# Kernel optimization log

Hardware: AMD Instinct MI355X
Metric: run time of the kernel (lower is better)

## Reference

```python
import jax, jax.numpy as jnp
import numpy as np

N, NFEAT, NHID, NCLASS, NHEADS = 8192, 512, 64, 16, 4
ALPHA = 0.2          # leaky_relu slope for attention scores
OUT_SLOPE = 0.01     # flax default slope for per-head output leaky_relu
NEG = -9000000000000000.0


def glorot(key, shape):
    fan_in, fan_out = shape[0], shape[1]
    lim = jnp.sqrt(6.0 / (fan_in + fan_out))
    return jax.random.uniform(key, shape, jnp.float32, -lim, lim)


def setup_inputs() -> dict:
    key = jax.random.key(0)
    ks = jax.random.split(key, 6)
    x = jax.random.normal(ks[0], (N, NFEAT), jnp.float32)
    adj = jax.random.randint(ks[1], (N, N), 0, 2, jnp.int32)
    Wh = glorot(ks[2], (NHEADS * NFEAT, NHID)).reshape(NHEADS, NFEAT, NHID)
    ah = glorot(ks[3], (NHEADS * 2 * NHID, 1)).reshape(NHEADS, 2 * NHID, 1)
    Wo = glorot(ks[4], (NHID * NHEADS, NCLASS))
    ao = glorot(ks[5], (2 * NCLASS, 1))
    return {"x": x, "adj": adj, "Wh": Wh, "ah": ah, "Wo": Wo, "ao": ao}


def _gat_layer(x, adj_mask, W, a, score_slope):
    # h: (N, F)
    h = x @ W
    F = h.shape[1]
    # a_input[i,j] = concat(h_i, h_j); a_input @ a == f1[i] + f2[j]
    f1 = h @ a[:F, 0]   # (N,)
    f2 = h @ a[F:, 0]   # (N,)
    e = jax.nn.leaky_relu(f1[:, None] + f2[None, :], negative_slope=score_slope)
    att = jax.nn.softmax(jnp.where(adj_mask, e, NEG), axis=1)  # (N, N)
    return att @ h  # (N, F)


def reference(x, adj, Wh, ah, Wo, ao):
    adj_mask = adj > 0
    heads = []
    for k in range(NHEADS):  # small fixed structural loop
        hp = _gat_layer(x, adj_mask, Wh[k], ah[k], ALPHA)
        heads.append(jax.nn.leaky_relu(hp, negative_slope=OUT_SLOPE))
    xcat = jnp.concatenate(heads, axis=1)  # (N, NHEADS*NHID)
    # output head: concat=False -> return h_prime directly
    return _gat_layer(xcat, adj_mask, Wo, ao, ALPHA)  # (N, NCLASS)
```

## Files before the change

kernel.cpp:

```cpp
#include <hip/hip_runtime.h>
#include <stdint.h>

#define N      8192
#define FEAT   512
#define HID    64
#define NH     4
#define C1     256
#define PCH    65
#define TC     260
#define NCLS   16
#define C2     32
#define IPB    8
#define LOG2E  1.44269504f

typedef __attribute__((ext_vector_type(8))) short bf16x8;
typedef __attribute__((ext_vector_type(4))) float f32x4;

__device__ __forceinline__ float b2f(uint16_t u){
  uint32_t x = ((uint32_t)u) << 16;
  return __builtin_bit_cast(float, x);
}
__device__ __forceinline__ uint16_t f2b(float f){
  uint32_t x = __builtin_bit_cast(uint32_t, f);
  uint32_t r = (x + 0x7fffu + ((x >> 16) & 1u)) >> 16;
  return (uint16_t)r;
}
__device__ __forceinline__ float lrelu(float v, float a){ return fmaxf(v, a * v); }
__device__ __forceinline__ float fexp2(float x){
#if __has_builtin(__builtin_amdgcn_exp2f)
  return __builtin_amdgcn_exp2f(x);
#else
  return exp2f(x);
#endif
}
__device__ __forceinline__ uint32_t pk_bf16(float lo, float hi){
  uint32_t r;
  asm("v_cvt_pk_bf16_f32 %0, %1, %2" : "=v"(r) : "v"(lo), "v"(hi));
  return r;
}

__device__ __forceinline__ bf16x8 mk_frag(float f1v, float4 fa, float4 fb,
                                          uint32_t ub, float& dsum){
  float e0, e1, e2, e3, e4, e5, e6, e7, s;
  s = f1v + fa.x; e0 = fexp2(fmaxf(s, 0.2f * s)); if (!(ub &   1u)) e0 = 0.f;
  s = f1v + fa.y; e1 = fexp2(fmaxf(s, 0.2f * s)); if (!(ub &   2u)) e1 = 0.f;
  s = f1v + fa.z; e2 = fexp2(fmaxf(s, 0.2f * s)); if (!(ub &   4u)) e2 = 0.f;
  s = f1v + fa.w; e3 = fexp2(fmaxf(s, 0.2f * s)); if (!(ub &   8u)) e3 = 0.f;
  s = f1v + fb.x; e4 = fexp2(fmaxf(s, 0.2f * s)); if (!(ub &  16u)) e4 = 0.f;
  s = f1v + fb.y; e5 = fexp2(fmaxf(s, 0.2f * s)); if (!(ub &  32u)) e5 = 0.f;
  s = f1v + fb.z; e6 = fexp2(fmaxf(s, 0.2f * s)); if (!(ub &  64u)) e6 = 0.f;
  s = f1v + fb.w; e7 = fexp2(fmaxf(s, 0.2f * s)); if (!(ub & 128u)) e7 = 0.f;
  dsum += ((e0 + e1) + (e2 + e3)) + ((e4 + e5) + (e6 + e7));
  union { uint32_t u[4]; bf16x8 v; } r;
  r.u[0] = pk_bf16(e0, e1);
  r.u[1] = pk_bf16(e2, e3);
  r.u[2] = pk_bf16(e4, e5);
  r.u[3] = pk_bf16(e6, e7);
  return r.v;
}

#define MFMA16(a, b, c) __builtin_amdgcn_mfma_f32_16x16x32_bf16((a), (b), (c), 0, 0, 0)

__global__ __launch_bounds__(256) void kp_pack(const int* __restrict__ adj,
                                               uint32_t* __restrict__ adjT){
  __shared__ uint32_t tile[2][64];
  int t = threadIdx.x, lane = t & 63, wv = t >> 6;
  int jt = blockIdx.x & 127;
  int i0 = (blockIdx.x >> 7) * 64;
  const int j0 = jt * 64;
  #pragma unroll
  for (int r = 0; r < 16; ++r){
    int row = wv * 16 + r;
    unsigned long long mb = __ballot(adj[(size_t)(i0 + row) * N + j0 + lane] > 0);
    if (lane == 0){
      tile[0][row] = (uint32_t)mb;
      tile[1][row] = (uint32_t)(mb >> 32);
    }
  }
  __syncthreads();
  if (t < 128){
    int ww = t >> 6, r = t & 63;
    adjT[(size_t)(jt * 2 + ww) * N + i0 + r] = tile[ww][r];
  }
}

__global__ __launch_bounds__(256) void k1_h(const float* __restrict__ x,
    const float* __restrict__ Wh, const float* __restrict__ ah,
    uint16_t* __restrict__ H, float* __restrict__ f1, float* __restrict__ f2)
{
  int t = threadIdx.x;
  int i0 = blockIdx.x * IPB;
  int k = t >> 6, cc = t & 63;
  const float* wcol = Wh + k * 32768 + cc;
  float acc[IPB] = {};
  for (int f = 0; f < FEAT; f += 4){
    float w0 = wcol[(f + 0) * 64];
    float w1 = wcol[(f + 1) * 64];
    float w2 = wcol[(f + 2) * 64];
    float w3 = wcol[(f + 3) * 64];
    #pragma unroll
    for (int ii = 0; ii < IPB; ++ii){
      const float* xr = x + (size_t)(i0 + ii) * FEAT + f;
      acc[ii] += xr[0] * w0 + xr[1] * w1 + xr[2] * w2 + xr[3] * w3;
    }
  }
  float a1 = ah[k * 128 + cc], a2 = ah[k * 128 + 64 + cc];
  #pragma unroll
  for (int ii = 0; ii < IPB; ++ii){
    int i = i0 + ii;
    H[(size_t)i * C1 + t] = f2b(acc[ii]);
    float c1v = acc[ii] * a1, c2v = acc[ii] * a2;
    #pragma unroll
    for (int off = 32; off; off >>= 1){
      c1v += __shfl_down(c1v, off);
      c2v += __shfl_down(c2v, off);
    }
    if (cc == 0){ f1[k * N + i] = c1v * LOG2E; f2[k * N + i] = c2v * LOG2E; }
  }
}

__global__ void k2a_pack(const uint16_t* __restrict__ H, uint16_t* __restrict__ Bp){
  __shared__ uint16_t tile[64][72];
  int bid = blockIdx.x;
  int k = bid & 3, it = bid >> 2;
  int i0 = it * 64;
  int t = threadIdx.x;
  #pragma unroll
  for (int r = 0; r < 4; ++r){
    int ii = r * 16 + (t >> 4);
    int pp = (t & 15) * 4;
    uint2 v = *(const uint2*)(H + (size_t)(i0 + ii) * C1 + k * 64 + pp);
    const uint16_t* s = (const uint16_t*)&v;
    tile[pp + 0][ii] = s[0]; tile[pp + 1][ii] = s[1];
    tile[pp + 2][ii] = s[2]; tile[pp + 3][ii] = s[3];
  }
  __syncthreads();
  #pragma unroll
  for (int r = 0; r < 2; ++r){
    int jl = r;
    int ct = t >> 6;
    int lane = t & 63;
    int m = lane & 15, q = lane >> 4;
    uint4 v = *(const uint4*)&tile[ct * 16 + m][jl * 32 + q * 8];
    size_t off = ((((size_t)k * 256 + (i0 >> 5) + jl) * 4 + ct) * 64 + lane) * 8;
    *(uint4*)(Bp + off) = v;
  }
}

#define K3_LOADB(BD, JC)                                                        \
  { const int jb = (JC) & 63;                                                   \
    _Pragma("unroll")                                                           \
    for (int ct = 0; ct < 4; ++ct)                                              \
      BD[ct] = *(const bf16x8*)(bpbase + (size_t)(jb * 4 + ct) * 512); }

#define K3_LOADWF(W0d, W1d, F0d, F1d, JC)                                       \
  { const int jw = (JC) & 63;                                                   \
    W0d = adjT[awbase + (size_t)jw * N];                                        \
    W1d = adjT[awbase + (size_t)jw * N + 16];                                   \
    F0d = *(const float4*)(f2js + jw * 32 + 8 * q);                             \
    F1d = *(const float4*)(f2js + jw * 32 + 8 * q + 4); }

#define K3_COMP(BU, W0u, W1u, F0u, F1u)                                         \
  { bf16x8 af0 = mk_frag(f1v0, F0u, F1u, (W0u >> (8 * q)) & 255u, dsum0);       \
    bf16x8 af1 = mk_frag(f1v1, F0u, F1u, (W1u >> (8 * q)) & 255u, dsum1);       \
    _Pragma("unroll")                                                           \
    for (int ct = 0; ct < 4; ++ct){                                             \
      acc[0][ct] = MFMA16(af0, BU[ct], acc[0][ct]);                             \
      acc[1][ct] = MFMA16(af1, BU[ct], acc[1][ct]);                             \
    } }

#define K3_STEP(BU, BL, JB, U, L, JW)                                           \
  { K3_LOADB(BL, JB);                                                           \
    K3_LOADWF(w##L##0, w##L##1, f##L##0, f##L##1, JW);                          \
    K3_COMP(BU, w##U##0, w##U##1, f##U##0, f##U##1) }

__global__ __launch_bounds__(256, 4) void k3_attA(const uint32_t* __restrict__ adjT,
    const uint16_t* __restrict__ Bp, const float* __restrict__ f1,
    const float* __restrict__ f2, float* __restrict__ accA)
{
  const int t = threadIdx.x;
  const int ibl = blockIdx.x & 255;
  const int js  = blockIdx.x >> 8;
  const int gi0 = ibl * 32;

  const int lane = t & 63;
  const int head = t >> 6;
  const int m    = lane & 15;
  const int q    = lane >> 4;

  const int row0  = gi0 + m;
  const float* f2js = f2 + (size_t)head * N + js * 2048;
  const float f1v0 = f1[(size_t)head * N + row0];
  const float f1v1 = f1[(size_t)head * N + row0 + 16];
  const uint16_t* bpbase = Bp + (((size_t)head * 256 + js * 64) * 4) * 512 + lane * 8;
  const size_t awbase = (size_t)(js * 64) * N + row0;

  f32x4 acc[2][4] = {};
  float dsum0 = 0.f, dsum1 = 0.f;

  bf16x8 b0[4], b1[4], b2[4];
  uint32_t wA0, wA1, wB0, wB1;
  float4 fA0, fA1, fB0, fB1;

  K3_LOADB(b0, 0)
  K3_LOADB(b1, 1)
  K3_LOADWF(wA0, wA1, fA0, fA1, 0)

  for (int i = 0; i < 10; ++i){
    const int kb = i * 6;
    K3_STEP(b0, b2, kb + 2, A, B, kb + 1)
    K3_STEP(b1, b0, kb + 3, B, A, kb + 2)
    K3_STEP(b2, b1, kb + 4, A, B, kb + 3)
    K3_STEP(b0, b2, kb + 5, B, A, kb + 4)
    K3_STEP(b1, b0, kb + 6, A, B, kb + 5)
    K3_STEP(b2, b1, kb + 7, B, A, kb + 6)
  }
  K3_STEP(b0, b2, 62, A, B, 61)
  K3_STEP(b1, b0, 63, B, A, 62)
  K3_STEP(b2, b1, 64, A, B, 63)
  K3_STEP(b0, b2, 65, B, A, 64)

  #pragma unroll
  for (int itl = 0; itl < 2; ++itl)
    #pragma unroll
    for (int ct = 0; ct < 4; ++ct)
      #pragma unroll
      for (int reg = 0; reg < 4; ++reg){
        int gi = gi0 + itl * 16 + q * 4 + reg;
        accA[((size_t)js * N + gi) * TC + head * PCH + ct * 16 + m] = acc[itl][ct][reg];
      }
  {
    float v0 = dsum0, v1 = dsum1;
    v0 += __shfl_xor(v0, 16); v0 += __shfl_xor(v0, 32);
    v1 += __shfl_xor(v1, 16); v1 += __shfl_xor(v1, 32);
    if (q == 0){
      accA[((size_t)js * N + row0)      * TC + head * PCH + 64] = v0;
      accA[((size_t)js * N + row0 + 16) * TC + head * PCH + 64] = v1;
    }
  }
}

__global__ void k4_redA(const float* __restrict__ accA, uint16_t* __restrict__ xcat){
  int i = blockIdx.x;
  int t = threadIdx.x;
  int k = t >> 6, cc = t & 63;
  size_t base = (size_t)i * TC + k * PCH;
  float v = 0.f, Z = 0.f;
  #pragma unroll
  for (int js = 0; js < 4; ++js){
    const float* p = accA + (size_t)js * N * TC + base;
    v += p[cc];
    Z += p[64];
  }
  float r = v / Z;
  xcat[(size_t)i * C1 + t] = f2b(lrelu(r, 0.01f));
}

__global__ __launch_bounds__(256) void k5_h2(const uint16_t* __restrict__ xcat,
    const float* __restrict__ Wo, const float* __restrict__ ao,
    uint16_t* __restrict__ Bp2, float* __restrict__ f1o, float* __restrict__ f2o)
{
  __shared__ uint16_t xs[16][256];
  __shared__ uint16_t hs[16][16];
  int t = threadIdx.x;
  int i0 = blockIdx.x * 16;
  #pragma unroll
  for (int r = 0; r < 2; ++r){
    int idx = t + 256 * r;
    int ii = idx >> 5, o4 = idx & 31;
    *(uint4*)&xs[ii][o4 * 8] = *(const uint4*)(xcat + (size_t)(i0 + ii) * C1 + o4 * 8);
  }
  __syncthreads();
  int ii = t >> 4, c = t & 15;
  float acc = 0.f;
  for (int f = 0; f < 256; ++f)
    acc += b2f(xs[ii][f]) * Wo[f * 16 + c];
  int i = i0 + ii;
  hs[ii][c] = f2b(acc);
  float u1 = acc * ao[c];
  float u2 = acc * ao[16 + c];
  #pragma unroll
  for (int off = 8; off; off >>= 1){
    u1 += __shfl_down(u1, off, 16);
    u2 += __shfl_down(u2, off, 16);
  }
  if (c == 0){ f1o[i] = u1 * LOG2E; f2o[i] = u2 * LOG2E; }
  __syncthreads();
  if (t < 32){
    int q_l = t >> 4, mm = t & 15;
    uint16_t tmp[8];
    #pragma unroll
    for (int s = 0; s < 8; ++s) tmp[s] = hs[8 * q_l + s][mm];
    int jcg = i0 >> 5, half = (i0 >> 4) & 1;
    size_t off = ((size_t)jcg * 64 + (2 * half + q_l) * 16 + mm) * 8;
    *(uint4*)(Bp2 + off) = *(uint4*)tmp;
  }
}

#define K6_BODY(JC, CUR, NXT)                                                   \
  {                                                                             \
    const int jcn = ((JC) + 1) & 31;                                            \
    b##NXT = *(const bf16x8*)(bp2 + (size_t)jcn * 512);                         \
    w##NXT = adjT[(size_t)(js * 32 + jcn) * N + row];                           \
    f##NXT##0 = *(const float4*)(f2o + js * 1024 + jcn * 32 + 8 * q);           \
    f##NXT##1 = *(const float4*)(f2o + js * 1024 + jcn * 32 + 8 * q + 4);       \
    bf16x8 af = mk_frag(f1v, f##CUR##0, f##CUR##1,                              \
                        (w##CUR >> (8 * q)) & 255u, dsum);                      \
    acc0 = MFMA16(af, b##CUR, acc0);                                            \
  }

__global__ __launch_bounds__(256, 4) void k6_attB(const uint32_t* __restrict__ adjT,
    const uint16_t* __restrict__ Bp2, const float* __restrict__ f1o,
    const float* __restrict__ f2o, float* __restrict__ accB)
{
  const int t = threadIdx.x;
  const int ibl = blockIdx.x & 127;
  const int js  = blockIdx.x >> 7;
  const int gi0 = ibl * 64;

  const int lane = t & 63;
  const int w = t >> 6;
  const int m = lane & 15;
  const int q = lane >> 4;

  const int row = gi0 + w * 16 + m;
  const float f1v = f1o[row];
  const uint16_t* bp2 = Bp2 + ((size_t)js * 32 * 64) * 8 + lane * 8;

  f32x4 acc0 = {0.f, 0.f, 0.f, 0.f};
  float dsum = 0.f;

  bf16x8 bA, bB;
  uint32_t wA, wB;
  float4 fA0, fA1, fB0, fB1;

  {
    bA = *(const bf16x8*)(bp2);
    wA = adjT[(size_t)(js * 32) * N + row];
    fA0 = *(const float4*)(f2o + js * 1024 + 8 * q);
    fA1 = *(const float4*)(f2o + js * 1024 + 8 * q + 4);
  }

  for (int jc = 0; jc < 32; jc += 2){
    K6_BODY(jc,     A, B)
    K6_BODY(jc + 1, B, A)
  }

  #pragma unroll
  for (int reg = 0; reg < 4; ++reg){
    int gi = gi0 + w * 16 + q * 4 + reg;
    accB[((size_t)js * N + gi) * C2 + m] = acc0[reg];
  }
  {
    float v = dsum;
    v += __shfl_xor(v, 16); v += __shfl_xor(v, 32);
    if (q == 0)
      accB[((size_t)js * N + row) * C2 + 16] = v;
  }
}

__global__ void k7_redB(const float* __restrict__ accB, float* __restrict__ out){
  int idx = blockIdx.x * 256 + threadIdx.x;
  int i = idx >> 4, c = idx & 15;
  float v = 0.f, Z = 0.f;
  #pragma unroll
  for (int js = 0; js < 8; ++js){
    const float* p = accB + ((size_t)js * N + i) * C2;
    v += p[c];
    Z += p[16];
  }
  out[idx] = v / Z;
}

extern "C" void kernel_launch(void* const* d_in, const int* in_sizes, int n_in,
                              void* d_out, int out_size, void* d_ws, size_t ws_size,
                              hipStream_t stream)
{
  const float* x   = (const float*)d_in[0];
  const int*   adj = (const int*)d_in[1];
  const float* Wh  = (const float*)d_in[2];
  const float* ah  = (const float*)d_in[3];
  const float* Wo  = (const float*)d_in[4];
  const float* ao  = (const float*)d_in[5];
  float* out = (float*)d_out;

  char* ws = (char*)d_ws;
  uint16_t* H    = (uint16_t*)(ws);
  uint16_t* Bp   = (uint16_t*)(ws + 4194304);
  float*    f1   = (float*)   (ws + 8388608);
  float*    f2   = (float*)   (ws + 8519680);
  float*    accA = (float*)   (ws + 8650752);
  uint16_t* xcat = (uint16_t*)(ws + 42729472);
  uint16_t* Bp2  = (uint16_t*)(ws + 46923776);
  float*    f1o  = (float*)   (ws + 47185920);
  float*    f2o  = (float*)   (ws + 47218688);
  float*    accB = (float*)   (ws + 47251456);
  uint32_t* adjT = (uint32_t*)(ws + 55640064);

  hipLaunchKernelGGL(kp_pack,  dim3(16384), dim3(256), 0, stream, adj, adjT);
  hipLaunchKernelGGL(k1_h,     dim3(1024),  dim3(256), 0, stream, x, Wh, ah, H, f1, f2);
  hipLaunchKernelGGL(k2a_pack, dim3(512),   dim3(256), 0, stream, H, Bp);
  hipLaunchKernelGGL(k3_attA,  dim3(1024),  dim3(256), 0, stream, adjT, Bp, f1, f2, accA);
  hipLaunchKernelGGL(k4_redA,  dim3(8192),  dim3(256), 0, stream, accA, xcat);
  hipLaunchKernelGGL(k5_h2,    dim3(512),   dim3(256), 0, stream, xcat, Wo, ao, Bp2, f1o, f2o);
  hipLaunchKernelGGL(k6_attB,  dim3(1024),  dim3(256), 0, stream, adjT, Bp2, f1o, f2o, accB);
  hipLaunchKernelGGL(k7_redB,  dim3(512),   dim3(256), 0, stream, accB, out);
}
```

Before: 693.5 us.

## Fuse split-K partial reductions into attention kernels via shared memory

The attention kernels now use 1024-thread blocks. Each block covers 16 rows and all column splits, and the waves combine their partial numerators and softmax denominators in shared memory. The separate reduction kernels and their large fp32 partial-sum buffers in global memory are removed, along with two launches. In exchange, each block handles fewer rows, so adjacency and B-fragment loads are no longer amortised over 32 rows. The software-pipelined register prefetch is also replaced by a plain loop, which may expose memory latency.

```diff
diff --git a/kernel.cpp b/kernel.cpp
--- a/kernel.cpp
+++ b/kernel.cpp
@@ -6,10 +6,7 @@
 #define HID    64
 #define NH     4
 #define C1     256
-#define PCH    65
-#define TC     260
 #define NCLS   16
-#define C2     32
 #define IPB    8
 #define LOG2E  1.44269504f
 
@@ -147,113 +144,75 @@
   }
 }
 
-#define K3_LOADB(BD, JC)                                                        \
-  { const int jb = (JC) & 63;                                                   \
-    _Pragma("unroll")                                                           \
-    for (int ct = 0; ct < 4; ++ct)                                              \
-      BD[ct] = *(const bf16x8*)(bpbase + (size_t)(jb * 4 + ct) * 512); }
-
-#define K3_LOADWF(W0d, W1d, F0d, F1d, JC)                                       \
-  { const int jw = (JC) & 63;                                                   \
-    W0d = adjT[awbase + (size_t)jw * N];                                        \
-    W1d = adjT[awbase + (size_t)jw * N + 16];                                   \
-    F0d = *(const float4*)(f2js + jw * 32 + 8 * q);                             \
-    F1d = *(const float4*)(f2js + jw * 32 + 8 * q + 4); }
-
-#define K3_COMP(BU, W0u, W1u, F0u, F1u)                                         \
-  { bf16x8 af0 = mk_frag(f1v0, F0u, F1u, (W0u >> (8 * q)) & 255u, dsum0);       \
-    bf16x8 af1 = mk_frag(f1v1, F0u, F1u, (W1u >> (8 * q)) & 255u, dsum1);       \
-    _Pragma("unroll")                                                           \
-    for (int ct = 0; ct < 4; ++ct){                                             \
-      acc[0][ct] = MFMA16(af0, BU[ct], acc[0][ct]);                             \
-      acc[1][ct] = MFMA16(af1, BU[ct], acc[1][ct]);                             \
-    } }
-
-#define K3_STEP(BU, BL, JB, U, L, JW)                                           \
-  { K3_LOADB(BL, JB);                                                           \
-    K3_LOADWF(w##L##0, w##L##1, f##L##0, f##L##1, JW);                          \
-    K3_COMP(BU, w##U##0, w##U##1, f##U##0, f##U##1) }
-
-__global__ __launch_bounds__(256, 4) void k3_attA(const uint32_t* __restrict__ adjT,
+__global__ __launch_bounds__(1024, 8) void k3_attA(const uint32_t* __restrict__ adjT,
     const uint16_t* __restrict__ Bp, const float* __restrict__ f1,
-    const float* __restrict__ f2, float* __restrict__ accA)
-{
+    const float* __restrict__ f2, uint16_t* __restrict__ xcat)
+{
+  __shared__ float red[3][4][64][17];
+  __shared__ float zred[4][4][16];
+  __shared__ float zfin[4][16];
+
   const int t = threadIdx.x;
-  const int ibl = blockIdx.x & 255;
-  const int js  = blockIdx.x >> 8;
-  const int gi0 = ibl * 32;
-
+  const int gi0 = blockIdx.x * 16;
   const int lane = t & 63;
-  const int head = t >> 6;
-  const int m    = lane & 15;
-  const int q    = lane >> 4;
-
-  const int row0  = gi0 + m;
-  const float* f2js = f2 + (size_t)head * N + js * 2048;
-  const float f1v0 = f1[(size_t)head * N + row0];
-  const float f1v1 = f1[(size_t)head * N + row0 + 16];
-  const uint16_t* bpbase = Bp + (((size_t)head * 256 + js * 64) * 4) * 512 + lane * 8;
-  const size_t awbase = (size_t)(js * 64) * N + row0;
-
-  f32x4 acc[2][4] = {};
-  float dsum0 = 0.f, dsum1 = 0.f;
-
-  bf16x8 b0[4], b1[4], b2[4];
-  uint32_t wA0, wA1, wB0, wB1;
-  float4 fA0, fA1, fB0, fB1;
-
-  K3_LOADB(b0, 0)
-  K3_LOADB(b1, 1)
-  K3_LOADWF(wA0, wA1, fA0, fA1, 0)
-
-  for (int i = 0; i < 10; ++i){
-    const int kb = i * 6;
-    K3_STEP(b0, b2, kb + 2, A, B, kb + 1)
-    K3_STEP(b1, b0, kb + 3, B, A, kb + 2)
-    K3_STEP(b2, b1, kb + 4, A, B, kb + 3)
-    K3_STEP(b0, b2, kb + 5, B, A, kb + 4)
-    K3_STEP(b1, b0, kb + 6, A, B, kb + 5)
-    K3_STEP(b2, b1, kb + 7, B, A, kb + 6)
-  }
-  K3_STEP(b0, b2, 62, A, B, 61)
-  K3_STEP(b1, b0, 63, B, A, 62)
-  K3_STEP(b2, b1, 64, A, B, 63)
-  K3_STEP(b0, b2, 65, B, A, 64)
-
-  #pragma unroll
-  for (int itl = 0; itl < 2; ++itl)
+  const int wv = t >> 6;
+  const int head = wv & 3;
+  const int jq = wv >> 2;
+  const int m = lane & 15;
+  const int q = lane >> 4;
+
+  const float* f2js = f2 + (size_t)head * N + jq * 2048;
+  const float f1v = f1[(size_t)head * N + gi0 + m];
+  const uint16_t* bpbase = Bp + (((size_t)head * 256 + jq * 64) * 4) * 512 + (size_t)lane * 8;
+  const uint32_t* aw = adjT + (size_t)(jq * 64) * N + gi0 + m;
+
+  f32x4 acc[4] = {};
+  float dsum = 0.f;
+
+  for (int jc = 0; jc < 64; ++jc){
+    bf16x8 b[4];
+    #pragma unroll
+    for (int ct = 0; ct < 4; ++ct)
+      b[ct] = *(const bf16x8*)(bpbase + (size_t)(jc * 4 + ct) * 512);
+    uint32_t wb = aw[(size_t)jc * N];
+    float4 fa = *(const float4*)(f2js + jc * 32 + 8 * q);
+    float4 fb = *(const float4*)(f2js + jc * 32 + 8 * q + 4);
+    bf16x8 af = mk_frag(f1v, fa, fb, (wb >> (8 * q)) & 255u, dsum);
+    #pragma unroll
+    for (int ct = 0; ct < 4; ++ct)
+      acc[ct] = MFMA16(af, b[ct], acc[ct]);
+  }
+
+  dsum += __shfl_xor(dsum, 16);
+  dsum += __shfl_xor(dsum, 32);
+  if (q == 0) zred[jq][head][m] = dsum;
+  if (jq != 0){
+    #pragma unroll
+    for (int ct = 0; ct < 4; ++ct)
+      #pragma unroll
+      for (int reg = 0; reg < 4; ++reg)
+        red[jq - 1][head][lane][ct * 4 + reg] = acc[ct][reg];
+  }
+  __syncthreads();
+  if (t < 64){
+    int h = t >> 4, r = t & 15;
+    zfin[h][r] = ((zred[0][h][r] + zred[1][h][r]) + (zred[2][h][r] + zred[3][h][r]));
+  }
+  __syncthreads();
+  if (jq == 0){
+    float zv[4];
+    #pragma unroll
+    for (int reg = 0; reg < 4; ++reg) zv[reg] = zfin[head][q * 4 + reg];
     #pragma unroll
     for (int ct = 0; ct < 4; ++ct)
       #pragma unroll
       for (int reg = 0; reg < 4; ++reg){
-        int gi = gi0 + itl * 16 + q * 4 + reg;
-        accA[((size_t)js * N + gi) * TC + head * PCH + ct * 16 + m] = acc[itl][ct][reg];
+        float v = acc[ct][reg] + red[0][head][lane][ct * 4 + reg]
+                + red[1][head][lane][ct * 4 + reg] + red[2][head][lane][ct * 4 + reg];
+        float r2 = v / zv[reg];
+        xcat[(size_t)(gi0 + q * 4 + reg) * C1 + head * 64 + ct * 16 + m] = f2b(lrelu(r2, 0.01f));
       }
-  {
-    float v0 = dsum0, v1 = dsum1;
-    v0 += __shfl_xor(v0, 16); v0 += __shfl_xor(v0, 32);
-    v1 += __shfl_xor(v1, 16); v1 += __shfl_xor(v1, 32);
-    if (q == 0){
-      accA[((size_t)js * N + row0)      * TC + head * PCH + 64] = v0;
-      accA[((size_t)js * N + row0 + 16) * TC + head * PCH + 64] = v1;
-    }
-  }
-}
-
-__global__ void k4_redA(const float* __restrict__ accA, uint16_t* __restrict__ xcat){
-  int i = blockIdx.x;
-  int t = threadIdx.x;
-  int k = t >> 6, cc = t & 63;
-  size_t base = (size_t)i * TC + k * PCH;
-  float v = 0.f, Z = 0.f;
-  #pragma unroll
-  for (int js = 0; js < 4; ++js){
-    const float* p = accA + (size_t)js * N * TC + base;
-    v += p[cc];
-    Z += p[64];
-  }
-  float r = v / Z;
-  xcat[(size_t)i * C1 + t] = f2b(lrelu(r, 0.01f));
+  }
 }
 
 __global__ __launch_bounds__(256) void k5_h2(const uint16_t* __restrict__ xcat,
@@ -297,79 +256,62 @@
   }
 }
 
-#define K6_BODY(JC, CUR, NXT)                                                   \
-  {                                                                             \
-    const int jcn = ((JC) + 1) & 31;                                            \
-    b##NXT = *(const bf16x8*)(bp2 + (size_t)jcn * 512);                         \
-    w##NXT = adjT[(size_t)(js * 32 + jcn) * N + row];                           \
-    f##NXT##0 = *(const float4*)(f2o + js * 1024 + jcn * 32 + 8 * q);           \
-    f##NXT##1 = *(const float4*)(f2o + js * 1024 + jcn * 32 + 8 * q + 4);       \
-    bf16x8 af = mk_frag(f1v, f##CUR##0, f##CUR##1,                              \
-                        (w##CUR >> (8 * q)) & 255u, dsum);                      \
-    acc0 = MFMA16(af, b##CUR, acc0);                                            \
-  }
-
-__global__ __launch_bounds__(256, 4) void k6_attB(const uint32_t* __restrict__ adjT,
+__global__ __launch_bounds__(1024, 8) void k6_attB(const uint32_t* __restrict__ adjT,
     const uint16_t* __restrict__ Bp2, const float* __restrict__ f1o,
-    const float* __restrict__ f2o, float* __restrict__ accB)
-{
+    const float* __restrict__ f2o, float* __restrict__ out)
+{
+  __shared__ float red[15][64][5];
+  __shared__ float zredB[16][16];
+
   const int t = threadIdx.x;
-  const int ibl = blockIdx.x & 127;
-  const int js  = blockIdx.x >> 7;
-  const int gi0 = ibl * 64;
-
+  const int gi0 = blockIdx.x * 16;
   const int lane = t & 63;
-  const int w = t >> 6;
+  const int wv = t >> 6;
   const int m = lane & 15;
   const int q = lane >> 4;
 
-  const int row = gi0 + w * 16 + m;
-  const float f1v = f1o[row];
-  const uint16_t* bp2 = Bp2 + ((size_t)js * 32 * 64) * 8 + lane * 8;
-
-  f32x4 acc0 = {0.f, 0.f, 0.f, 0.f};
+  const float f1v = f1o[gi0 + m];
+  const uint16_t* bp2 = Bp2 + (size_t)(wv * 16) * 512 + (size_t)lane * 8;
+  const uint32_t* aw = adjT + (size_t)(wv * 16) * N + gi0 + m;
+  const float* f2js = f2o + wv * 512;
+
+  f32x4 acc = {0.f, 0.f, 0.f, 0.f};
   float dsum = 0.f;
 
-  bf16x8 bA, bB;
-  uint32_t wA, wB;
-  float4 fA0, fA1, fB0, fB1;
-
-  {
-    bA = *(const bf16x8*)(bp2);
-    wA = adjT[(size_t)(js * 32) * N + row];
-    fA0 = *(const float4*)(f2o + js * 1024 + 8 * q);
-    fA1 = *(const float4*)(f2o + js * 1024 + 8 * q + 4);
-  }
-
-  for (int jc = 0; jc < 32; jc += 2){
-    K6_BODY(jc,     A, B)
-    K6_BODY(jc + 1, B, A)
-  }
-
-  #pragma unroll
-  for (int reg = 0; reg < 4; ++reg){
-    int gi = gi0 + w * 16 + q * 4 + reg;
-    accB[((size_t)js * N + gi) * C2 + m] = acc0[reg];
-  }
-  {
-    float v = dsum;
-    v += __shfl_xor(v, 16); v += __shfl_xor(v, 32);
-    if (q == 0)
-      accB[((size_t)js * N + row) * C2 + 16] = v;
-  }
-}
-
-__global__ void k7_redB(const float* __restrict__ accB, float* __restrict__ out){
-  int idx = blockIdx.x * 256 + threadIdx.x;
-  int i = idx >> 4, c = idx & 15;
-  float v = 0.f, Z = 0.f;
-  #pragma unroll
-  for (int js = 0; js < 8; ++js){
-    const float* p = accB + ((size_t)js * N + i) * C2;
-    v += p[c];
-    Z += p[16];
-  }
-  out[idx] = v / Z;
+  for (int jc = 0; jc < 16; ++jc){
+    bf16x8 b = *(const bf16x8*)(bp2 + (size_t)jc * 512);
+    uint32_t wb = aw[(size_t)jc * N];
+    float4 fa = *(const float4*)(f2js + jc * 32 + 8 * q);
+    float4 fb = *(const float4*)(f2js + jc * 32 + 8 * q + 4);
+    bf16x8 af = mk_frag(f1v, fa, fb, (wb >> (8 * q)) & 255u, dsum);
+    acc = MFMA16(af, b, acc);
+  }
+
+  dsum += __shfl_xor(dsum, 16);
+  dsum += __shfl_xor(dsum, 32);
+  if (q == 0) zredB[wv][m] = dsum;
+  if (wv != 0){
+    #pragma unroll
+    for (int reg = 0; reg < 4; ++reg) red[wv - 1][lane][reg] = acc[reg];
+  }
+  __syncthreads();
+  if (wv == 0){
+    float zv[4];
+    #pragma unroll
+    for (int reg = 0; reg < 4; ++reg){
+      float z = 0.f;
+      #pragma unroll
+      for (int k2 = 0; k2 < 16; ++k2) z += zredB[k2][q * 4 + reg];
+      zv[reg] = z;
+    }
+    #pragma unroll
+    for (int reg = 0; reg < 4; ++reg){
+      float v = acc[reg];
+      #pragma unroll
+      for (int k2 = 0; k2 < 15; ++k2) v += red[k2][lane][reg];
+      out[(size_t)(gi0 + q * 4 + reg) * NCLS + m] = v / zv[reg];
+    }
+  }
 }
 
 extern "C" void kernel_launch(void* const* d_in, const int* in_sizes, int n_in,
@@ -389,20 +331,16 @@
   uint16_t* Bp   = (uint16_t*)(ws + 4194304);
   float*    f1   = (float*)   (ws + 8388608);
   float*    f2   = (float*)   (ws + 8519680);
-  float*    accA = (float*)   (ws + 8650752);
-  uint16_t* xcat = (uint16_t*)(ws + 42729472);
-  uint16_t* Bp2  = (uint16_t*)(ws + 46923776);
-  float*    f1o  = (float*)   (ws + 47185920);
-  float*    f2o  = (float*)   (ws + 47218688);
-  float*    accB = (float*)   (ws + 47251456);
-  uint32_t* adjT = (uint32_t*)(ws + 55640064);
-
-  hipLaunchKernelGGL(kp_pack,  dim3(16384), dim3(256), 0, stream, adj, adjT);
-  hipLaunchKernelGGL(k1_h,     dim3(1024),  dim3(256), 0, stream, x, Wh, ah, H, f1, f2);
-  hipLaunchKernelGGL(k2a_pack, dim3(512),   dim3(256), 0, stream, H, Bp);
-  hipLaunchKernelGGL(k3_attA,  dim3(1024),  dim3(256), 0, stream, adjT, Bp, f1, f2, accA);
-  hipLaunchKernelGGL(k4_redA,  dim3(8192),  dim3(256), 0, stream, accA, xcat);
-  hipLaunchKernelGGL(k5_h2,    dim3(512),   dim3(256), 0, stream, xcat, Wo, ao, Bp2, f1o, f2o);
-  hipLaunchKernelGGL(k6_attB,  dim3(1024),  dim3(256), 0, stream, adjT, Bp2, f1o, f2o, accB);
-  hipLaunchKernelGGL(k7_redB,  dim3(512),   dim3(256), 0, stream, accB, out);
-}
+  uint16_t* xcat = (uint16_t*)(ws + 8650752);
+  uint16_t* Bp2  = (uint16_t*)(ws + 12845056);
+  float*    f1o  = (float*)   (ws + 13107200);
+  float*    f2o  = (float*)   (ws + 13139968);
+  uint32_t* adjT = (uint32_t*)(ws + 13172736);
+
+  hipLaunchKernelGGL(kp_pack,  dim3(16384), dim3(256),  0, stream, adj, adjT);
+  hipLaunchKernelGGL(k1_h,     dim3(1024),  dim3(256),  0, stream, x, Wh, ah, H, f1, f2);
+  hipLaunchKernelGGL(k2a_pack, dim3(512),   dim3(256),  0, stream, H, Bp);
+  hipLaunchKernelGGL(k3_attA,  dim3(512),   dim3(1024), 0, stream, adjT, Bp, f1, f2, xcat);
+  hipLaunchKernelGGL(k5_h2,    dim3(512),   dim3(256),  0, stream, xcat, Wo, ao, Bp2, f1o, f2o);
+  hipLaunchKernelGGL(k6_attB,  dim3(512),   dim3(1024), 0, stream, adjT, Bp2, f1o, f2o, out);
+}
```

Measured after the change: 636.1 us. 1.09x faster.
